# Kernel optimization log

Hardware: AMD Instinct MI355X
Metric: run time of the kernel (lower is better)

The kernel has to match this reference:

```python
import jax, jax.numpy as jnp
import numpy as np

N = 16384
F_IN = 128
F_OUT = 128


def setup_inputs() -> dict:
    key = jax.random.key(0)
    k1, k2, k3, k4 = jax.random.split(key, 4)
    Adjacency = jax.random.uniform(k1, (N, N), dtype=jnp.float32)
    Features = jax.random.normal(k2, (N, F_IN), dtype=jnp.float32)
    W = jax.random.normal(k3, (F_OUT, F_IN), dtype=jnp.float32) * (1.0 / np.sqrt(F_IN))
    b = jax.random.normal(k4, (F_OUT,), dtype=jnp.float32) * 0.01
    return {"Adjacency": Adjacency, "Features": Features, "W": W, "b": b}


def reference(Adjacency, Features, W, b):
    # normalization = row_sum^{-1/2}, inf (zero-degree) -> 0
    deg = Adjacency.sum(axis=1)                      # [N]
    norm = jnp.where(deg > 0, deg ** -0.5, 0.0)      # [N]
    # A_hat = D^{-1/2} A D^{-1/2}
    A_hat = Adjacency * norm[:, None] * norm[None, :]
    agg = A_hat @ Features                           # [N, F_IN]
    return agg @ W.T + b                             # [N, F_OUT]
```

## Files before the change

### kernel.cpp

```cpp
#include <hip/hip_runtime.h>
#include <stdint.h>

#define NN 16384
#define FD 128

typedef float f32x4 __attribute__((ext_vector_type(4)));
typedef float f32x16 __attribute__((ext_vector_type(16)));
typedef __bf16 bf16x8 __attribute__((ext_vector_type(8)));
typedef unsigned short u16x8 __attribute__((ext_vector_type(8)));
typedef unsigned short u16x4 __attribute__((ext_vector_type(4)));

static __device__ __forceinline__ unsigned short f2bf(float x) {
  return __builtin_bit_cast(unsigned short, (__bf16)x);
}

static __device__ __forceinline__ u16x8 pack8(f32x4 a, f32x4 b) {
  u16x8 r;
  r[0] = f2bf(a.x); r[1] = f2bf(a.y); r[2] = f2bf(a.z); r[3] = f2bf(a.w);
  r[4] = f2bf(b.x); r[5] = f2bf(b.y); r[6] = f2bf(b.z); r[7] = f2bf(b.w);
  return r;
}

static __device__ __forceinline__ u16x4 pack4(f32x4 a) {
  u16x4 r;
  r[0] = f2bf(a.x); r[1] = f2bf(a.y); r[2] = f2bf(a.z); r[3] = f2bf(a.w);
  return r;
}

__global__ __launch_bounds__(256) void k_rownorm(const float* __restrict__ A,
                                                 float* __restrict__ norm) {
  const int row = blockIdx.x;
  const f32x4* ar = (const f32x4*)(A + (size_t)row * NN);
  float s = 0.f;
#pragma unroll 4
  for (int c = threadIdx.x; c < NN / 4; c += 256) {
    f32x4 v = __builtin_nontemporal_load(&ar[c]);
    s += (v.x + v.y) + (v.z + v.w);
  }
#pragma unroll
  for (int off = 32; off > 0; off >>= 1) s += __shfl_xor(s, off, 64);
  __shared__ float red[4];
  const int lane = threadIdx.x & 63, w = threadIdx.x >> 6;
  if (lane == 0) red[w] = s;
  __syncthreads();
  if (threadIdx.x == 0) {
    float d = (red[0] + red[1]) + (red[2] + red[3]);
    norm[row] = d > 0.f ? 1.f / sqrtf(d) : 0.f;
  }
}

__global__ __launch_bounds__(256) void k_fwt(const float* __restrict__ F,
                                             const float* __restrict__ W,
                                             const float* __restrict__ norm,
                                             unsigned short* __restrict__ Bfrag) {
  const int tid = threadIdx.x;
  const int wv = tid >> 6;
  const int l = tid & 63;
  const int lr = l & 31, lg = l >> 5;
  const int j0 = blockIdx.x * 32;

  const float* fp = F + (size_t)(j0 + lr) * FD + lg * 8;
  const float* wp = W + (size_t)(wv * 32 + lr) * FD + lg * 8;

  f32x16 acc;
#pragma unroll
  for (int i = 0; i < 16; ++i) acc[i] = 0.f;

#pragma unroll
  for (int kf = 0; kf < 8; ++kf) {
    f32x4 fa = *(const f32x4*)(fp + kf * 16);
    f32x4 fb = *(const f32x4*)(fp + kf * 16 + 4);
    f32x4 wa = *(const f32x4*)(wp + kf * 16);
    f32x4 wb = *(const f32x4*)(wp + kf * 16 + 4);
    bf16x8 av = __builtin_bit_cast(bf16x8, pack8(fa, fb));
    bf16x8 bv = __builtin_bit_cast(bf16x8, pack8(wa, wb));
    acc = __builtin_amdgcn_mfma_f32_32x32x16_bf16(av, bv, acc, 0, 0, 0);
  }

  const int jt = blockIdx.x * 2;
#pragma unroll
  for (int g = 0; g < 4; ++g) {
    const int jb = j0 + g * 8 + lg * 4;
    u16x4 q;
#pragma unroll
    for (int r2 = 0; r2 < 4; ++r2) q[r2] = f2bf(acc[g * 4 + r2] * norm[jb + r2]);
    const size_t byteoff =
        ((size_t)((jt + (g >> 1)) * 4 + wv) * 64 + (g & 1) * 32 + lr) * 16 +
        lg * 8;
    *(u16x4*)((char*)Bfrag + byteoff) = q;
  }
}

__global__ __launch_bounds__(1024, 4) void k_gcn_gemm(
    const float* __restrict__ A, const unsigned short* __restrict__ Bfrag,
    const float* __restrict__ norm, const float* __restrict__ bias,
    float* __restrict__ out) {
  __shared__ __align__(16) unsigned short Alds[2][64 * 256];

  const int tid = threadIdx.x;
  const int i0 = blockIdx.x * 64;

  const int srow = tid >> 6;
  const int sl = tid & 63;
  const float* aptr = A + (size_t)(i0 + srow) * NN + (size_t)sl * 4;
  const unsigned abase =
      (unsigned)(srow * 512) + ((unsigned)(sl * 8) ^ (unsigned)(srow << 4));

  const int wv = tid >> 6;
  const int c = wv & 3;
  const int m = (wv >> 2) & 1;
  const int kg = wv >> 3;
  const int l = tid & 63;
  const int lr = l & 31, lg = l >> 5;
  const int rowl = m * 32 + lr;
  const unsigned swz = (unsigned)((rowl & 15) << 4);
  const unsigned arb = (unsigned)(rowl * 512);
  const unsigned kgb = (unsigned)(kg * 256);

  const char* bptr = (const char*)Bfrag + (size_t)(c * 64 + l) * 16 +
                     (size_t)kg * 8 * 4096;

  f32x16 acc;
#pragma unroll
  for (int i = 0; i < 16; ++i) acc[i] = 0.f;

#define ALOAD(RV, S, I)                                                     \
  RV = __builtin_nontemporal_load(                                          \
      (const f32x4*)(aptr + (size_t)(S) * 256 + (size_t)(I) * (16 * NN)));
#define AWRITE(BUF, RV, I)                                                  \
  *(u16x4*)((char*)Alds[BUF] + (abase + (I) * 8192)) = pack4(RV);

  {
    f32x4 r0, r1, r2, r3;
    ALOAD(r0, 0, 0) ALOAD(r1, 0, 1) ALOAD(r2, 0, 2) ALOAD(r3, 0, 3)
    AWRITE(0, r0, 0) AWRITE(0, r1, 1) AWRITE(0, r2, 2) AWRITE(0, r3, 3)
  }
  __syncthreads();

#define GSTEP(CUR, NXT, S)                                                  \
  {                                                                         \
    const int s_ = (S);                                                     \
    const bool pf_ = (s_ + 1) < 64;                                         \
    f32x4 r0 = {}, r1 = {}, r2 = {}, r3 = {};                               \
    if (pf_) {                                                              \
      ALOAD(r0, s_ + 1, 0) ALOAD(r1, s_ + 1, 1)                             \
      ALOAD(r2, s_ + 1, 2) ALOAD(r3, s_ + 1, 3)                             \
    }                                                                       \
    const char* bp_ = bptr + (size_t)s_ * (16 * 4096);                      \
    _Pragma("unroll") for (int kf = 0; kf < 8; ++kf) {                      \
      u16x8 bv = *(const u16x8*)(bp_ + (size_t)kf * 4096);                  \
      unsigned ko = (kgb + (unsigned)(kf * 32) + (unsigned)(lg * 16)) ^ swz;\
      u16x8 av = *(const u16x8*)((const char*)Alds[CUR] + (arb + ko));      \
      acc = __builtin_amdgcn_mfma_f32_32x32x16_bf16(                        \
          __builtin_bit_cast(bf16x8, av), __builtin_bit_cast(bf16x8, bv),   \
          acc, 0, 0, 0);                                                    \
    }                                                                       \
    if (pf_) {                                                              \
      AWRITE(NXT, r0, 0) AWRITE(NXT, r1, 1)                                 \
      AWRITE(NXT, r2, 2) AWRITE(NXT, r3, 3)                                 \
    }                                                                       \
    __syncthreads();                                                        \
  }

#pragma unroll 1
  for (int s = 0; s < 64; s += 2) {
    GSTEP(0, 1, s)
    GSTEP(1, 0, s + 1)
  }
#undef GSTEP
#undef ALOAD
#undef AWRITE

  float* red = (float*)Alds;
  if (kg == 1) {
#pragma unroll
    for (int g = 0; g < 4; ++g) {
      const int jb = m * 32 + g * 8 + lg * 4;
#pragma unroll
      for (int r2 = 0; r2 < 4; ++r2)
        red[(jb + r2) * 128 + c * 32 + lr] = acc[g * 4 + r2];
    }
  }
  __syncthreads();
  if (kg == 0) {
#pragma unroll
    for (int g = 0; g < 4; ++g) {
      const int jb = m * 32 + g * 8 + lg * 4;
#pragma unroll
      for (int r2 = 0; r2 < 4; ++r2)
        red[(jb + r2) * 128 + c * 32 + lr] += acc[g * 4 + r2];
    }
  }
  __syncthreads();

  {
    const int row = tid >> 4;
    const int colseg = (tid & 15) * 8;
    const float nm = norm[i0 + row];
    f32x4 v0 = *(const f32x4*)(red + row * 128 + colseg);
    f32x4 v1 = *(const f32x4*)(red + row * 128 + colseg + 4);
    f32x4 b0 = *(const f32x4*)(bias + colseg);
    f32x4 b1 = *(const f32x4*)(bias + colseg + 4);
    f32x4 o0, o1;
    o0.x = nm * v0.x + b0.x; o0.y = nm * v0.y + b0.y;
    o0.z = nm * v0.z + b0.z; o0.w = nm * v0.w + b0.w;
    o1.x = nm * v1.x + b1.x; o1.y = nm * v1.y + b1.y;
    o1.z = nm * v1.z + b1.z; o1.w = nm * v1.w + b1.w;
    float* op = out + (size_t)(i0 + row) * FD + colseg;
    *(f32x4*)op = o0;
    *(f32x4*)(op + 4) = o1;
  }
}

extern "C" void kernel_launch(void* const* d_in, const int* in_sizes, int n_in,
                              void* d_out, int out_size, void* d_ws,
                              size_t ws_size, hipStream_t stream) {
  (void)in_sizes; (void)n_in; (void)out_size; (void)ws_size;
  const float* A = (const float*)d_in[0];
  const float* F = (const float*)d_in[1];
  const float* W = (const float*)d_in[2];
  const float* b = (const float*)d_in[3];
  float* out = (float*)d_out;

  float* norm = (float*)d_ws;
  unsigned short* Bfrag = (unsigned short*)((char*)d_ws + 65536);

  k_rownorm<<<NN, 256, 0, stream>>>(A, norm);
  k_fwt<<<NN / 32, 256, 0, stream>>>(F, W, norm, Bfrag);
  k_gcn_gemm<<<NN / 64, 1024, 0, stream>>>(A, Bfrag, norm, b, out);
}
```

Baseline: 393.4 us.

## Deepen A-tile prefetch to two stages and use lightweight LDS-only barriers

The main GEMM loop now keeps two register sets of A prefetches in flight, loading the tile two steps ahead instead of one. This gives global loads more time to land before their LDS write. Full __syncthreads is replaced by an lgkmcnt wait plus s_barrier, so outstanding global loads are not drained at each barrier. The rownorm pass switches from nontemporal to normal loads, possibly so A rows stay in cache for the GEMM. The extra in-flight registers may raise register pressure at 1024 threads per block.

```diff
diff --git a/kernel.cpp b/kernel.cpp
--- a/kernel.cpp
+++ b/kernel.cpp
@@ -34,7 +34,7 @@
   float s = 0.f;
 #pragma unroll 4
   for (int c = threadIdx.x; c < NN / 4; c += 256) {
-    f32x4 v = __builtin_nontemporal_load(&ar[c]);
+    f32x4 v = ar[c];
     s += (v.x + v.y) + (v.z + v.w);
   }
 #pragma unroll
@@ -124,29 +124,22 @@
 #pragma unroll
   for (int i = 0; i < 16; ++i) acc[i] = 0.f;
 
+  f32x4 a0, a1, a2, a3, b0, b1, b2, b3;
+
 #define ALOAD(RV, S, I)                                                     \
   RV = __builtin_nontemporal_load(                                          \
       (const f32x4*)(aptr + (size_t)(S) * 256 + (size_t)(I) * (16 * NN)));
 #define AWRITE(BUF, RV, I)                                                  \
   *(u16x4*)((char*)Alds[BUF] + (abase + (I) * 8192)) = pack4(RV);
-
-  {
-    f32x4 r0, r1, r2, r3;
-    ALOAD(r0, 0, 0) ALOAD(r1, 0, 1) ALOAD(r2, 0, 2) ALOAD(r3, 0, 3)
-    AWRITE(0, r0, 0) AWRITE(0, r1, 1) AWRITE(0, r2, 2) AWRITE(0, r3, 3)
-  }
-  __syncthreads();
-
-#define GSTEP(CUR, NXT, S)                                                  \
+#define BARR                                                                \
+  do {                                                                      \
+    asm volatile("s_waitcnt lgkmcnt(0)" ::: "memory");                      \
+    __builtin_amdgcn_s_barrier();                                           \
+    __builtin_amdgcn_sched_barrier(0);                                      \
+  } while (0)
+#define MFMA_BLOCK(CUR, S)                                                  \
   {                                                                         \
-    const int s_ = (S);                                                     \
-    const bool pf_ = (s_ + 1) < 64;                                         \
-    f32x4 r0 = {}, r1 = {}, r2 = {}, r3 = {};                               \
-    if (pf_) {                                                              \
-      ALOAD(r0, s_ + 1, 0) ALOAD(r1, s_ + 1, 1)                             \
-      ALOAD(r2, s_ + 1, 2) ALOAD(r3, s_ + 1, 3)                             \
-    }                                                                       \
-    const char* bp_ = bptr + (size_t)s_ * (16 * 4096);                      \
+    const char* bp_ = bptr + (size_t)(S) * (16 * 4096);                     \
     _Pragma("unroll") for (int kf = 0; kf < 8; ++kf) {                      \
       u16x8 bv = *(const u16x8*)(bp_ + (size_t)kf * 4096);                  \
       unsigned ko = (kgb + (unsigned)(kf * 32) + (unsigned)(lg * 16)) ^ swz;\
@@ -155,19 +148,38 @@
           __builtin_bit_cast(bf16x8, av), __builtin_bit_cast(bf16x8, bv),   \
           acc, 0, 0, 0);                                                    \
     }                                                                       \
-    if (pf_) {                                                              \
-      AWRITE(NXT, r0, 0) AWRITE(NXT, r1, 1)                                 \
-      AWRITE(NXT, r2, 2) AWRITE(NXT, r3, 3)                                 \
-    }                                                                       \
-    __syncthreads();                                                        \
-  }
+  }
+
+  ALOAD(a0, 0, 0) ALOAD(a1, 0, 1) ALOAD(a2, 0, 2) ALOAD(a3, 0, 3)
+  ALOAD(b0, 1, 0) ALOAD(b1, 1, 1) ALOAD(b2, 1, 2) ALOAD(b3, 1, 3)
+  AWRITE(0, a0, 0) AWRITE(0, a1, 1) AWRITE(0, a2, 2) AWRITE(0, a3, 3)
+  BARR;
 
 #pragma unroll 1
   for (int s = 0; s < 64; s += 2) {
-    GSTEP(0, 1, s)
-    GSTEP(1, 0, s + 1)
-  }
-#undef GSTEP
+    {
+      if (s + 2 < 64) {
+        ALOAD(a0, s + 2, 0) ALOAD(a1, s + 2, 1)
+        ALOAD(a2, s + 2, 2) ALOAD(a3, s + 2, 3)
+      }
+      MFMA_BLOCK(0, s)
+      AWRITE(1, b0, 0) AWRITE(1, b1, 1) AWRITE(1, b2, 2) AWRITE(1, b3, 3)
+      BARR;
+    }
+    {
+      if (s + 3 < 64) {
+        ALOAD(b0, s + 3, 0) ALOAD(b1, s + 3, 1)
+        ALOAD(b2, s + 3, 2) ALOAD(b3, s + 3, 3)
+      }
+      MFMA_BLOCK(1, s + 1)
+      if (s + 2 < 64) {
+        AWRITE(0, a0, 0) AWRITE(0, a1, 1) AWRITE(0, a2, 2) AWRITE(0, a3, 3)
+      }
+      BARR;
+    }
+  }
+#undef MFMA_BLOCK
+#undef BARR
 #undef ALOAD
 #undef AWRITE
 
@@ -199,13 +211,13 @@
     const float nm = norm[i0 + row];
     f32x4 v0 = *(const f32x4*)(red + row * 128 + colseg);
     f32x4 v1 = *(const f32x4*)(red + row * 128 + colseg + 4);
-    f32x4 b0 = *(const f32x4*)(bias + colseg);
-    f32x4 b1 = *(const f32x4*)(bias + colseg + 4);
+    f32x4 b0v = *(const f32x4*)(bias + colseg);
+    f32x4 b1v = *(const f32x4*)(bias + colseg + 4);
     f32x4 o0, o1;
-    o0.x = nm * v0.x + b0.x; o0.y = nm * v0.y + b0.y;
-    o0.z = nm * v0.z + b0.z; o0.w = nm * v0.w + b0.w;
-    o1.x = nm * v1.x + b1.x; o1.y = nm * v1.y + b1.y;
-    o1.z = nm * v1.z + b1.z; o1.w = nm * v1.w + b1.w;
+    o0.x = nm * v0.x + b0v.x; o0.y = nm * v0.y + b0v.y;
+    o0.z = nm * v0.z + b0v.z; o0.w = nm * v0.w + b0v.w;
+    o1.x = nm * v1.x + b1v.x; o1.y = nm * v1.y + b1v.y;
+    o1.z = nm * v1.z + b1v.z; o1.w = nm * v1.w + b1v.w;
     float* op = out + (size_t)(i0 + row) * FD + colseg;
     *(f32x4*)op = o0;
     *(f32x4*)(op + 4) = o1;
```

Measured after the change: 395.8 us. About the same (+0.6%).
